# Optimization experiments

Hardware: AMD Instinct MI355X
Metric: run time of the kernel (lower is better)

The kernel has to match this reference:

```python
import jax, jax.numpy as jnp
import numpy as np

D_MODEL = 256; D_FC = 1024; N_LEVELS = 4; N_HEADS = 8; N_POINTS = 4
D_HEAD = D_MODEL // N_HEADS
SPATIAL = np.array([[100, 100], [50, 50], [25, 25], [13, 13]], dtype=np.int64)
S_TOTAL = int((SPATIAL[:, 0] * SPATIAL[:, 1]).sum())  # 13294
BATCH = 2


def setup_inputs() -> dict:
    key = jax.random.key(0)
    ks = jax.random.split(key, 16)

    def lin(k, fi, fo):
        s = 1.0 / np.sqrt(fi)
        kw, kb = jax.random.split(k)
        W = jax.random.uniform(kw, (fi, fo), jnp.float32, -s, s)
        b = jax.random.uniform(kb, (fo,), jnp.float32, -s, s)
        return W, b

    W_off, b_off = lin(ks[0], D_MODEL, N_HEADS * N_LEVELS * N_POINTS * 2)
    W_attn, b_attn = lin(ks[1], D_MODEL, N_HEADS * N_LEVELS * N_POINTS)
    W_val, b_val = lin(ks[2], D_MODEL, D_MODEL)
    W_out, b_out = lin(ks[3], D_MODEL, D_MODEL)
    W1, b1 = lin(ks[4], D_MODEL, D_FC)
    W2, b2 = lin(ks[5], D_FC, D_MODEL)
    src = jax.random.normal(ks[6], (BATCH, S_TOTAL, D_MODEL), jnp.float32)
    pos = jax.random.normal(ks[7], (BATCH, S_TOTAL, D_MODEL), jnp.float32)
    reference_points = jax.random.uniform(ks[8], (BATCH, S_TOTAL, N_LEVELS, 2), jnp.float32)
    level_start_index = np.concatenate([[0], np.cumsum(SPATIAL[:, 0] * SPATIAL[:, 1])[:-1]]).astype(np.int64)
    return dict(src=src, pos=pos, reference_points=reference_points,
                spatial_shapes=SPATIAL, level_start_index=level_start_index,
                W_off=W_off, b_off=b_off, W_attn=W_attn, b_attn=b_attn,
                W_val=W_val, b_val=b_val, W_out=W_out, b_out=b_out,
                ln1_g=jnp.ones(D_MODEL, jnp.float32), ln1_b=jnp.zeros(D_MODEL, jnp.float32),
                W1=W1, b1=b1, W2=W2, b2=b2,
                ln2_g=jnp.ones(D_MODEL, jnp.float32), ln2_b=jnp.zeros(D_MODEL, jnp.float32))


def layernorm(x, g, b, eps=1e-5):
    mu = x.mean(-1, keepdims=True)
    var = ((x - mu) ** 2).mean(-1, keepdims=True)
    return (x - mu) * jax.lax.rsqrt(var + eps) * g + b


def ms_deform_attn(query, value_in, ref_pts, shapes,
                   W_off, b_off, W_attn, b_attn, W_val, b_val, W_out, b_out):
    N, Lq, _ = query.shape
    value = (value_in @ W_val + b_val).reshape(N, -1, N_HEADS, D_HEAD)
    off = (query @ W_off + b_off).reshape(N, Lq, N_HEADS, N_LEVELS, N_POINTS, 2)
    attn = (query @ W_attn + b_attn).reshape(N, Lq, N_HEADS, N_LEVELS * N_POINTS)
    attn = jax.nn.softmax(attn, -1).reshape(N, Lq, N_HEADS, N_LEVELS, N_POINTS)
    # offset normalizer is (W_l, H_l) per level
    norm = jnp.array([[w, h] for (h, w) in shapes], dtype=query.dtype)
    loc = ref_pts[:, :, None, :, None, :] + off / norm[None, None, None, :, None, :]
    out = jnp.zeros((N, Lq, N_HEADS, D_HEAD), query.dtype)
    start = 0
    for l, (H_, W_) in enumerate(shapes):
        v = value[:, start:start + H_ * W_].transpose(0, 2, 1, 3)  # [N, heads, HW, d]
        start += H_ * W_
        loc_l = loc[:, :, :, l]  # [N, Lq, heads, P, 2]
        # grid_sample(align_corners=False, padding_mode='zeros'): pixel = loc*size - 0.5
        px = loc_l[..., 0] * W_ - 0.5
        py = loc_l[..., 1] * H_ - 0.5
        x0 = jnp.floor(px); y0 = jnp.floor(py)
        wx = (px - x0)[..., None]; wy = (py - y0)[..., None]
        x0i = x0.astype(jnp.int32); y0i = y0.astype(jnp.int32)

        def samp(xi, yi):
            valid = (xi >= 0) & (xi < W_) & (yi >= 0) & (yi < H_)
            idx = jnp.clip(yi, 0, H_ - 1) * W_ + jnp.clip(xi, 0, W_ - 1)  # [N,Lq,heads,P]
            idx = idx.transpose(0, 2, 1, 3).reshape(N, N_HEADS, Lq * N_POINTS, 1)
            g = jnp.take_along_axis(v, idx, axis=2)  # [N,heads,Lq*P,d]
            g = g.reshape(N, N_HEADS, Lq, N_POINTS, D_HEAD).transpose(0, 2, 1, 3, 4)
            return g * valid[..., None]

        val = (samp(x0i, y0i) * (1 - wx) * (1 - wy)
               + samp(x0i + 1, y0i) * wx * (1 - wy)
               + samp(x0i, y0i + 1) * (1 - wx) * wy
               + samp(x0i + 1, y0i + 1) * wx * wy)  # [N,Lq,heads,P,d]
        out = out + (val * attn[:, :, :, l, :, None]).sum(3)
    return out.reshape(N, Lq, D_MODEL) @ W_out + b_out


def reference(src, pos, reference_points, spatial_shapes, level_start_index,
              W_off, b_off, W_attn, b_attn, W_val, b_val, W_out, b_out,
              ln1_g, ln1_b, W1, b1, W2, b2, ln2_g, ln2_b):
    shapes = [(int(spatial_shapes[l, 0]), int(spatial_shapes[l, 1])) for l in range(N_LEVELS)]
    q = src + pos
    attn_out = ms_deform_attn(q, src, reference_points, shapes,
                              W_off, b_off, W_attn, b_attn, W_val, b_val, W_out, b_out)
    x = layernorm(src + attn_out, ln1_g, ln1_b)  # dropout is identity in eval
    ffn = jax.nn.relu(x @ W1 + b1) @ W2 + b2
    return layernorm(x + ffn, ln2_g, ln2_b)
```

## Files before the change

kernel.cpp:

```cpp
#include <hip/hip_runtime.h>
#include <hip/hip_bf16.h>

#define DM 256
#define STOT 13294
#define MTOT (2 * STOT)

using bf16 = __hip_bfloat16;
typedef __attribute__((ext_vector_type(8))) short short8;
typedef __attribute__((ext_vector_type(4))) float floatx4;

#define GLDS16(g, l) __builtin_amdgcn_global_load_lds( \
    (const __attribute__((address_space(1))) void*)(g), \
    (__attribute__((address_space(3))) void*)(l), 16, 0, 0)

__device__ __forceinline__ float bu2f(unsigned u) { return __uint_as_float(u << 16); }
__device__ __forceinline__ unsigned short f2bu(float f) {
    union { bf16 h; unsigned short u; } c; c.h = __float2bfloat16(f); return c.u;
}

__global__ void detect_dtype(const unsigned* g1, int* flag) {
    if (threadIdx.x == 0 && blockIdx.x == 0)
        *flag = (g1[0] == 0x3F800000u) ? 1 : 0;
}

struct PW { const void* W[6]; const void* B[10]; };

__global__ void prep_weights(PW a, bf16* __restrict__ WT, float* __restrict__ bf,
                             const int* __restrict__ flag) {
    const long id = (long)blockIdx.x * 256 + threadIdx.x;
    const bool f32in = (*flag != 0);
    const int sz[6]  = {65536, 65536, 32768, 65536, 262144, 262144};
    const int Ns[6]  = {256, 256, 128, 256, 1024, 256};
    const int Ksh[6] = {8, 8, 8, 8, 8, 10};
    if (id < 753664) {
        long e = id; int j = 0;
        while (e >= sz[j]) { e -= sz[j]; ++j; }
        const int n = (int)(e >> Ksh[j]);
        const int k = (int)(e & ((1 << Ksh[j]) - 1));
        const size_t src = (size_t)k * Ns[j] + n;
        float v = f32in ? ((const float*)a.W[j])[src] : __bfloat162float(((const bf16*)a.W[j])[src]);
        WT[id] = __float2bfloat16(v);
    } else if (id < 753664 + 3200) {
        long e = id - 753664; int j = 0;
        const int bsz[10] = {256, 256, 128, 256, 1024, 256, 256, 256, 256, 256};
        while (e >= bsz[j]) { e -= bsz[j]; ++j; }
        float v = f32in ? ((const float*)a.B[j])[e] : __bfloat162float(((const bf16*)a.B[j])[e]);
        bf[id - 753664] = v;
    }
}

__global__ void prep_act(const void* __restrict__ src, const void* __restrict__ pos,
                         bf16* __restrict__ sbf, bf16* __restrict__ qbf,
                         const int* __restrict__ flag) {
    const long i = ((long)blockIdx.x * 256 + threadIdx.x) * 8;
    if (i >= (long)MTOT * DM) return;
    unsigned short ps[8], pq[8];
    if (*flag) {
        const float* s = (const float*)src + i;
        const float* p = (const float*)pos + i;
        float4 a0 = *(const float4*)s, a1 = *(const float4*)(s + 4);
        float4 b0 = *(const float4*)p, b1 = *(const float4*)(p + 4);
        const float av[8] = {a0.x, a0.y, a0.z, a0.w, a1.x, a1.y, a1.z, a1.w};
        const float bv[8] = {b0.x, b0.y, b0.z, b0.w, b1.x, b1.y, b1.z, b1.w};
#pragma unroll
        for (int j = 0; j < 8; ++j) { ps[j] = f2bu(av[j]); pq[j] = f2bu(av[j] + bv[j]); }
    } else {
        const unsigned short* s = (const unsigned short*)src + i;
        const unsigned short* p = (const unsigned short*)pos + i;
        uint4 a = *(const uint4*)s, b = *(const uint4*)p;
        const unsigned* ua = (const unsigned*)&a;
        const unsigned* ub = (const unsigned*)&b;
#pragma unroll
        for (int j = 0; j < 4; ++j) {
            float a0 = bu2f(ua[j] & 0xffffu), a1 = bu2f(ua[j] >> 16);
            float b0 = bu2f(ub[j] & 0xffffu), b1 = bu2f(ub[j] >> 16);
            ps[j * 2] = f2bu(a0); ps[j * 2 + 1] = f2bu(a1);
            pq[j * 2] = f2bu(a0 + b0); pq[j * 2 + 1] = f2bu(a1 + b1);
        }
    }
    *(uint4*)((unsigned short*)sbf + i) = *(const uint4*)ps;
    *(uint4*)((unsigned short*)qbf + i) = *(const uint4*)pq;
}

template<bool RELU>
__global__ __launch_bounds__(256, 4)
void gemm_bf16(const bf16* __restrict__ A0, const bf16* __restrict__ A1, int n_a0,
               const bf16* __restrict__ WT, const float* __restrict__ bias,
               bf16* __restrict__ C0, bf16* __restrict__ C1, bf16* __restrict__ C2,
               int M, int N, int K, int ldc0) {
    __shared__ __align__(16) bf16 sh[16384];
    const int t = threadIdx.x;
    const int wave = t >> 6, lane = t & 63;
    const int bm = blockIdx.y * 128, bn = blockIdx.x * 128;
    const bf16* __restrict__ A = (bn < n_a0) ? A0 : A1;
    const int wm = (wave >> 1) * 64, wn = (wave & 1) * 64;
    const int l15 = lane & 15, quad = lane >> 4;
    const int srow = lane >> 2, sko = (lane & 3) * 8;

    floatx4 acc[4][4];
#pragma unroll
    for (int i = 0; i < 4; ++i)
#pragma unroll
        for (int j = 0; j < 4; ++j) acc[i][j] = (floatx4)0.f;

    const int nb = K >> 5;
#pragma unroll
    for (int rh = 0; rh < 2; ++rh) {
        const int rbase = rh * 64 + wave * 16;
        const int gm = min(bm + rbase + srow, M - 1);
        GLDS16(A + (size_t)gm * K + sko, &sh[rbase * 32]);
        GLDS16(WT + (size_t)(bn + rbase + srow) * K + sko, &sh[8192 + rbase * 32]);
    }
    for (int i = 0; i < nb; ++i) {
        __syncthreads();
        if (i + 1 < nb) {
            const int k0 = (i + 1) << 5;
            const int bo = ((i + 1) & 1) * 4096;
#pragma unroll
            for (int rh = 0; rh < 2; ++rh) {
                const int rbase = rh * 64 + wave * 16;
                const int gm = min(bm + rbase + srow, M - 1);
                GLDS16(A + (size_t)gm * K + k0 + sko, &sh[bo + rbase * 32]);
                GLDS16(WT + (size_t)(bn + rbase + srow) * K + k0 + sko, &sh[8192 + bo + rbase * 32]);
            }
        }
        const int bo = (i & 1) * 4096;
        short8 af[4], bfr[4];
#pragma unroll
        for (int mi = 0; mi < 4; ++mi)
            af[mi] = *(const short8*)&sh[bo + (wm + mi * 16 + l15) * 32 + quad * 8];
#pragma unroll
        for (int nj = 0; nj < 4; ++nj)
            bfr[nj] = *(const short8*)&sh[8192 + bo + (wn + nj * 16 + l15) * 32 + quad * 8];
#pragma unroll
        for (int mi = 0; mi < 4; ++mi)
#pragma unroll
            for (int nj = 0; nj < 4; ++nj)
                acc[mi][nj] = __builtin_amdgcn_mfma_f32_16x16x32_bf16(bfr[nj], af[mi], acc[mi][nj], 0, 0, 0);
    }

    bf16* C = C0; int coloff = bn, ldc = ldc0;
    if (C1 != nullptr && bn >= 256) {
        if (C2 != nullptr && bn >= 512) { C = C2; coloff = bn - 512; ldc = 128; }
        else                            { C = C1; coloff = bn - 256; ldc = 256; }
    }
    float4 bv4[4];
#pragma unroll
    for (int nj = 0; nj < 4; ++nj)
        bv4[nj] = *(const float4*)&bias[bn + wn + nj * 16 + quad * 4];
#pragma unroll
    for (int mi = 0; mi < 4; ++mi) {
        const int gm = bm + wm + mi * 16 + l15;
        if (gm >= M) continue;
#pragma unroll
        for (int nj = 0; nj < 4; ++nj) {
            const float bb[4] = {bv4[nj].x, bv4[nj].y, bv4[nj].z, bv4[nj].w};
            unsigned short pk[4];
#pragma unroll
            for (int r = 0; r < 4; ++r) {
                float v = acc[mi][nj][r] + bb[r];
                if (RELU) v = fmaxf(v, 0.f);
                pk[r] = f2bu(v);
            }
            *(uint2*)&C[(size_t)gm * ldc + coloff + wn + nj * 16 + quad * 4] = *(const uint2*)pk;
        }
    }
}

__global__ void softmax16(bf16* __restrict__ a, int total) {
    const int i = blockIdx.x * 256 + threadIdx.x;
    if (i >= total) return;
    unsigned short* p = (unsigned short*)(a + (size_t)i * 16);
    uint4 r0 = *(const uint4*)p, r1 = *(const uint4*)(p + 8);
    float w[16];
    const unsigned* u0 = (const unsigned*)&r0;
    const unsigned* u1 = (const unsigned*)&r1;
#pragma unroll
    for (int j = 0; j < 4; ++j) {
        w[j * 2] = bu2f(u0[j] & 0xffffu); w[j * 2 + 1] = bu2f(u0[j] >> 16);
        w[8 + j * 2] = bu2f(u1[j] & 0xffffu); w[8 + j * 2 + 1] = bu2f(u1[j] >> 16);
    }
    float mx = -1e30f;
#pragma unroll
    for (int j = 0; j < 16; ++j) mx = fmaxf(mx, w[j]);
    float s = 0.f;
#pragma unroll
    for (int j = 0; j < 16; ++j) { w[j] = __expf(w[j] - mx); s += w[j]; }
    const float inv = 1.f / s;
    unsigned short pk[16];
#pragma unroll
    for (int j = 0; j < 16; ++j) pk[j] = f2bu(w[j] * inv);
    *(uint4*)p = *(const uint4*)pk;
    *(uint4*)(p + 8) = *(const uint4*)(pk + 8);
}

__device__ __forceinline__ void corner(const bf16* __restrict__ base, int xi, int yi,
                                       int W_, int H_, float wgt, float* acc) {
    const bool valid = (xi >= 0) & (xi < W_) & (yi >= 0) & (yi < H_);
    const int xc = min(max(xi, 0), W_ - 1);
    const int yc = min(max(yi, 0), H_ - 1);
    const ushort4 v = *(const ushort4*)(base + (size_t)(yc * W_ + xc) * DM);
    const float m = valid ? wgt : 0.f;
    acc[0] += m * bu2f(v.x); acc[1] += m * bu2f(v.y);
    acc[2] += m * bu2f(v.z); acc[3] += m * bu2f(v.w);
}

__global__ void deform_sample(const bf16* __restrict__ value, const bf16* __restrict__ off,
                              const bf16* __restrict__ attw, const void* __restrict__ refp,
                              bf16* __restrict__ out, const int* __restrict__ flag) {
    const int t = threadIdx.x;
    const int q = blockIdx.x * 4 + (t >> 6);
    const int ln = t & 63;
    const int h = ln >> 3, dg = ln & 7;
    const int b = (q >= STOT) ? 1 : 0;

    float w[16];
    {
        const unsigned short* wp = (const unsigned short*)(attw + (size_t)q * 128 + h * 16);
        uint4 r0 = *(const uint4*)wp, r1 = *(const uint4*)(wp + 8);
        const unsigned* u0 = (const unsigned*)&r0;
        const unsigned* u1 = (const unsigned*)&r1;
#pragma unroll
        for (int j = 0; j < 4; ++j) {
            w[j * 2] = bu2f(u0[j] & 0xffffu); w[j * 2 + 1] = bu2f(u0[j] >> 16);
            w[8 + j * 2] = bu2f(u1[j] & 0xffffu); w[8 + j * 2 + 1] = bu2f(u1[j] >> 16);
        }
    }
    float of[32];
    {
        const unsigned short* op = (const unsigned short*)(off + (size_t)q * 256 + h * 32);
#pragma unroll
        for (int c = 0; c < 4; ++c) {
            uint4 r = *(const uint4*)(op + c * 8);
            const unsigned* u = (const unsigned*)&r;
#pragma unroll
            for (int j = 0; j < 4; ++j) {
                of[c * 8 + j * 2] = bu2f(u[j] & 0xffffu);
                of[c * 8 + j * 2 + 1] = bu2f(u[j] >> 16);
            }
        }
    }
    float rxy[8];
    if (*flag) {
        const float* rp = (const float*)refp + (size_t)q * 8;
        float4 r0 = *(const float4*)rp, r1 = *(const float4*)(rp + 4);
        rxy[0] = r0.x; rxy[1] = r0.y; rxy[2] = r0.z; rxy[3] = r0.w;
        rxy[4] = r1.x; rxy[5] = r1.y; rxy[6] = r1.z; rxy[7] = r1.w;
    } else {
        const unsigned short* rp = (const unsigned short*)refp + (size_t)q * 8;
        uint4 r = *(const uint4*)rp;
        const unsigned* u = (const unsigned*)&r;
#pragma unroll
        for (int j = 0; j < 4; ++j) {
            rxy[j * 2] = bu2f(u[j] & 0xffffu); rxy[j * 2 + 1] = bu2f(u[j] >> 16);
        }
    }

    const int Hs4[4] = {100, 50, 25, 13};
    const int Ls[4] = {0, 10000, 12500, 13125};
    const bf16* vb = value + (size_t)(b * STOT) * DM + h * 32 + dg * 4;

    float acc[4] = {0.f, 0.f, 0.f, 0.f};
#pragma unroll
    for (int l = 0; l < 4; ++l) {
        const int W_ = Hs4[l], H_ = Hs4[l];
        const bf16* base = vb + (size_t)Ls[l] * DM;
        const float fw = (float)W_, fh = (float)H_;
#pragma unroll
        for (int p = 0; p < 4; ++p) {
            const float px = rxy[l * 2] * fw + of[(l * 4 + p) * 2] - 0.5f;
            const float py = rxy[l * 2 + 1] * fh + of[(l * 4 + p) * 2 + 1] - 0.5f;
            const float x0f = floorf(px), y0f = floorf(py);
            const float wx = px - x0f, wy = py - y0f;
            const int x0 = (int)x0f, y0 = (int)y0f;
            const float aw = w[l * 4 + p];
            const float ex = 1.f - wx, ey = 1.f - wy;
            corner(base, x0, y0, W_, H_, ex * ey * aw, acc);
            corner(base, x0 + 1, y0, W_, H_, wx * ey * aw, acc);
            corner(base, x0, y0 + 1, W_, H_, ex * wy * aw, acc);
            corner(base, x0 + 1, y0 + 1, W_, H_, wx * wy * aw, acc);
        }
    }
    unsigned short pk[4] = {f2bu(acc[0]), f2bu(acc[1]), f2bu(acc[2]), f2bu(acc[3])};
    *(ushort4*)((unsigned short*)out + (size_t)q * 256 + h * 32 + dg * 4) = *(const ushort4*)pk;
}

__global__ __launch_bounds__(512, 1)
void out_ln1(const bf16* __restrict__ vsamp, const bf16* __restrict__ srcbf,
             const bf16* __restrict__ WoT, const float* __restrict__ bo_f,
             const float* __restrict__ g1, const float* __restrict__ be1,
             bf16* __restrict__ vx, int M) {
    __shared__ __align__(16) bf16 Bs[8 * 4096];
    const int t = threadIdx.x, wave = t >> 6, lane = t & 63;
    const int l15 = lane & 15, quad = lane >> 4;
    const int srow = lane >> 2, sko = (lane & 3) * 8;
    const int bm = blockIdx.x * 128;
    const int mrow = bm + wave * 16 + l15;
    const int mc = min(mrow, M - 1);

    short8 af[8];
#pragma unroll
    for (int kk = 0; kk < 8; ++kk)
        af[kk] = *(const short8*)(vsamp + (size_t)mc * 256 + kk * 32 + quad * 8);

    floatx4 acc[16];
#pragma unroll
    for (int i = 0; i < 16; ++i) acc[i] = (floatx4)0.f;

    for (int nc = 0; nc < 2; ++nc) {
        __syncthreads();
#pragma unroll
        for (int rr = 0; rr < 8; ++rr)
            GLDS16(WoT + (size_t)(nc * 128 + rr * 16 + srow) * 256 + wave * 32 + sko,
                   &Bs[wave * 4096 + rr * 512]);
        __syncthreads();
#pragma unroll
        for (int kk = 0; kk < 8; ++kk)
#pragma unroll
            for (int nj = 0; nj < 8; ++nj) {
                short8 bfr = *(const short8*)&Bs[kk * 4096 + (nj * 16 + l15) * 32 + quad * 8];
                acc[nc * 8 + nj] = __builtin_amdgcn_mfma_f32_16x16x32_bf16(bfr, af[kk], acc[nc * 8 + nj], 0, 0, 0);
            }
    }

    float s = 0.f;
#pragma unroll
    for (int nj = 0; nj < 16; ++nj) {
        const int n = nj * 16 + quad * 4;
        const float4 bo = *(const float4*)&bo_f[n];
        const uint2 ru = *(const uint2*)(srcbf + (size_t)mc * 256 + n);
        const float rs[4] = {bu2f(ru.x & 0xffffu), bu2f(ru.x >> 16), bu2f(ru.y & 0xffffu), bu2f(ru.y >> 16)};
        const float bb[4] = {bo.x, bo.y, bo.z, bo.w};
#pragma unroll
        for (int r = 0; r < 4; ++r) { acc[nj][r] += bb[r] + rs[r]; s += acc[nj][r]; }
    }
    s += __shfl_xor(s, 16, 64); s += __shfl_xor(s, 32, 64);
    const float mean = s * (1.f / 256.f);
    float s2 = 0.f;
#pragma unroll
    for (int nj = 0; nj < 16; ++nj)
#pragma unroll
        for (int r = 0; r < 4; ++r) { const float c = acc[nj][r] - mean; s2 += c * c; }
    s2 += __shfl_xor(s2, 16, 64); s2 += __shfl_xor(s2, 32, 64);
    const float rstd = rsqrtf(s2 * (1.f / 256.f) + 1e-5f);
    if (mrow < M) {
#pragma unroll
        for (int nj = 0; nj < 16; ++nj) {
            const int n = nj * 16 + quad * 4;
            const float4 g = *(const float4*)&g1[n];
            const float4 b = *(const float4*)&be1[n];
            const float gg[4] = {g.x, g.y, g.z, g.w}, bb[4] = {b.x, b.y, b.z, b.w};
            unsigned short pk[4];
#pragma unroll
            for (int r = 0; r < 4; ++r) pk[r] = f2bu((acc[nj][r] - mean) * rstd * gg[r] + bb[r]);
            *(uint2*)&vx[(size_t)mrow * 256 + n] = *(const uint2*)pk;
        }
    }
}

__global__ __launch_bounds__(256, 2)
void ffn_ln2(const bf16* __restrict__ vx, const bf16* __restrict__ W1T, const bf16* __restrict__ W2T,
             const float* __restrict__ b1f, const float* __restrict__ b2f,
             const float* __restrict__ g2, const float* __restrict__ be2,
             void* __restrict__ outp, const int* __restrict__ flag, int M) {
    __shared__ __align__(16) bf16 Bs1[16384];
    __shared__ __align__(16) bf16 Bs2[8192];
    __shared__ __align__(16) bf16 Hs[64 * 136];
    __shared__ float2 red[128];
    const int t = threadIdx.x, wv = t >> 6, lane = t & 63;
    const int l15 = lane & 15, quad = lane >> 4;
    const int g = wv & 1, nh = wv >> 1;
    const int srow = lane >> 2, sko = (lane & 3) * 8;
    const int bm = blockIdx.x * 64;

    int mrow[2], mc[2];
#pragma unroll
    for (int mi = 0; mi < 2; ++mi) {
        mrow[mi] = bm + g * 32 + mi * 16 + l15;
        mc[mi] = min(mrow[mi], M - 1);
    }
    short8 af[2][8];
#pragma unroll
    for (int mi = 0; mi < 2; ++mi)
#pragma unroll
        for (int kk = 0; kk < 8; ++kk)
            af[mi][kk] = *(const short8*)(vx + (size_t)mc[mi] * 256 + kk * 32 + quad * 8);

    floatx4 acc2[2][8];
#pragma unroll
    for (int mi = 0; mi < 2; ++mi)
#pragma unroll
        for (int nj = 0; nj < 8; ++nj) acc2[mi][nj] = (floatx4)0.f;

    for (int ch = 0; ch < 8; ++ch) {
        floatx4 acc1[2][4];
#pragma unroll
        for (int mi = 0; mi < 2; ++mi)
#pragma unroll
            for (int nj = 0; nj < 4; ++nj) acc1[mi][nj] = (floatx4)0.f;
#pragma unroll
        for (int ks = 0; ks < 2; ++ks) {
            __syncthreads();
#pragma unroll
            for (int j = 0; j < 8; ++j)
                GLDS16(W1T + (size_t)(ch * 128 + j * 16 + srow) * 256 + ks * 128 + wv * 32 + sko,
                       &Bs1[wv * 4096 + j * 512]);
            __syncthreads();
#pragma unroll
            for (int kk = 0; kk < 4; ++kk) {
                short8 bfr[4];
#pragma unroll
                for (int nj = 0; nj < 4; ++nj)
                    bfr[nj] = *(const short8*)&Bs1[kk * 4096 + (nh * 64 + nj * 16 + l15) * 32 + quad * 8];
#pragma unroll
                for (int mi = 0; mi < 2; ++mi)
#pragma unroll
                    for (int nj = 0; nj < 4; ++nj)
                        acc1[mi][nj] = __builtin_amdgcn_mfma_f32_16x16x32_bf16(bfr[nj], af[mi][ks * 4 + kk], acc1[mi][nj], 0, 0, 0);
            }
        }
#pragma unroll
        for (int mi = 0; mi < 2; ++mi)
#pragma unroll
            for (int nj = 0; nj < 4; ++nj) {
                const int kl = nh * 64 + nj * 16 + quad * 4;
                const float4 bb = *(const float4*)&b1f[ch * 128 + kl];
                const float bv[4] = {bb.x, bb.y, bb.z, bb.w};
                unsigned short pk[4];
#pragma unroll
                for (int r = 0; r < 4; ++r) pk[r] = f2bu(fmaxf(acc1[mi][nj][r] + bv[r], 0.f));
                *(uint2*)&Hs[(g * 32 + mi * 16 + l15) * 136 + kl] = *(const uint2*)pk;
            }
#pragma unroll
        for (int p = 0; p < 4; ++p) {
            __syncthreads();
#pragma unroll
            for (int j = 0; j < 4; ++j)
                GLDS16(W2T + (size_t)(wv * 64 + j * 16 + srow) * 1024 + ch * 128 + p * 32 + sko,
                       &Bs2[(wv * 64 + j * 16) * 32]);
            __syncthreads();
            short8 ah[2];
#pragma unroll
            for (int mi = 0; mi < 2; ++mi)
                ah[mi] = *(const short8*)&Hs[(g * 32 + mi * 16 + l15) * 136 + p * 32 + quad * 8];
#pragma unroll
            for (int nj = 0; nj < 8; ++nj) {
                short8 bfr = *(const short8*)&Bs2[(nh * 128 + nj * 16 + l15) * 32 + quad * 8];
#pragma unroll
                for (int mi = 0; mi < 2; ++mi)
                    acc2[mi][nj] = __builtin_amdgcn_mfma_f32_16x16x32_bf16(bfr, ah[mi], acc2[mi][nj], 0, 0, 0);
            }
        }
    }

    float sm[2] = {0.f, 0.f}, sq[2] = {0.f, 0.f};
#pragma unroll
    for (int mi = 0; mi < 2; ++mi)
#pragma unroll
        for (int nj = 0; nj < 8; ++nj) {
            const int n = nh * 128 + nj * 16 + quad * 4;
            const float4 bo = *(const float4*)&b2f[n];
            const uint2 ru = *(const uint2*)(vx + (size_t)mc[mi] * 256 + n);
            const float rs[4] = {bu2f(ru.x & 0xffffu), bu2f(ru.x >> 16), bu2f(ru.y & 0xffffu), bu2f(ru.y >> 16)};
            const float bb[4] = {bo.x, bo.y, bo.z, bo.w};
#pragma unroll
            for (int r = 0; r < 4; ++r) {
                const float v = acc2[mi][nj][r] + bb[r] + rs[r];
                acc2[mi][nj][r] = v; sm[mi] += v; sq[mi] += v * v;
            }
        }
#pragma unroll
    for (int mi = 0; mi < 2; ++mi) {
        sm[mi] += __shfl_xor(sm[mi], 16, 64); sm[mi] += __shfl_xor(sm[mi], 32, 64);
        sq[mi] += __shfl_xor(sq[mi], 16, 64); sq[mi] += __shfl_xor(sq[mi], 32, 64);
    }
    __syncthreads();
    if (quad == 0) {
#pragma unroll
        for (int mi = 0; mi < 2; ++mi)
            red[((nh * 2 + g) * 2 + mi) * 16 + l15] = make_float2(sm[mi], sq[mi]);
    }
    __syncthreads();
    const bool f32o = (*flag != 0);
#pragma unroll
    for (int mi = 0; mi < 2; ++mi) {
        const float2 o = red[(((1 - nh) * 2 + g) * 2 + mi) * 16 + l15];
        const float ts = sm[mi] + o.x, tq = sq[mi] + o.y;
        const float mean = ts * (1.f / 256.f);
        const float var = tq * (1.f / 256.f) - mean * mean;
        const float rstd = rsqrtf(var + 1e-5f);
        if (mrow[mi] < M) {
#pragma unroll
            for (int nj = 0; nj < 8; ++nj) {
                const int n = nh * 128 + nj * 16 + quad * 4;
                const float4 gv = *(const float4*)&g2[n];
                const float4 bv = *(const float4*)&be2[n];
                const float gg[4] = {gv.x, gv.y, gv.z, gv.w}, bb[4] = {bv.x, bv.y, bv.z, bv.w};
                float y[4];
#pragma unroll
                for (int r = 0; r < 4; ++r) y[r] = (acc2[mi][nj][r] - mean) * rstd * gg[r] + bb[r];
                if (f32o) {
                    float4 ov = {y[0], y[1], y[2], y[3]};
                    *(float4*)((float*)outp + (size_t)mrow[mi] * 256 + n) = ov;
                } else {
                    unsigned short pk[4] = {f2bu(y[0]), f2bu(y[1]), f2bu(y[2]), f2bu(y[3])};
                    *(uint2*)((bf16*)outp + (size_t)mrow[mi] * 256 + n) = *(const uint2*)pk;
                }
            }
        }
    }
}

extern "C" void kernel_launch(void* const* d_in, const int* in_sizes, int n_in,
                              void* d_out, int out_size, void* d_ws, size_t ws_size,
                              hipStream_t stream) {
    const void* src   = d_in[0];
    const void* pos   = d_in[1];
    const void* refp  = d_in[2];
    const void* W_off = d_in[5];
    const void* b_off = d_in[6];
    const void* W_att = d_in[7];
    const void* b_att = d_in[8];
    const void* W_val = d_in[9];
    const void* b_val = d_in[10];
    const void* W_out = d_in[11];
    const void* b_out = d_in[12];
    const void* ln1g  = d_in[13];
    const void* ln1b  = d_in[14];
    const void* W1    = d_in[15];
    const void* b1    = d_in[16];
    const void* W2    = d_in[17];
    const void* b2    = d_in[18];
    const void* ln2g  = d_in[19];
    const void* ln2b  = d_in[20];

    const size_t M = MTOT;
    bf16* src_bf = (bf16*)d_ws;
    bf16* q_bf   = src_bf + M * 256;
    bf16* v_val  = src_bf + M * 512;
    bf16* v_off  = src_bf + M * 768;
    bf16* v_attn = src_bf + M * 1024;
    bf16* v_samp = src_bf + M * 1152;
    bf16* v_x    = src_bf + M * 1408;
    bf16* WT     = src_bf + M * 1664;
    float* biasf = (float*)(WT + 753664);
    int* flag    = (int*)(biasf + 3200);

    dim3 blk(256);
    const int mg = (MTOT + 127) / 128;

    detect_dtype<<<1, 64, 0, stream>>>((const unsigned*)ln1g, flag);

    PW pw;
    pw.W[0] = W_val; pw.W[1] = W_off; pw.W[2] = W_att; pw.W[3] = W_out; pw.W[4] = W1; pw.W[5] = W2;
    pw.B[0] = b_val; pw.B[1] = b_off; pw.B[2] = b_att; pw.B[3] = b_out; pw.B[4] = b1; pw.B[5] = b2;
    pw.B[6] = ln1g;  pw.B[7] = ln1b;  pw.B[8] = ln2g;  pw.B[9] = ln2b;
    prep_weights<<<(753664 + 3200 + 255) / 256, blk, 0, stream>>>(pw, WT, biasf, flag);
    prep_act<<<(int)((M * 256 / 8 + 255) / 256), blk, 0, stream>>>(src, pos, src_bf, q_bf, flag);

    gemm_bf16<false><<<dim3(5, mg), blk, 0, stream>>>(src_bf, q_bf, 256, WT, biasf,
                                                      v_val, v_off, v_attn, MTOT, 640, 256, 256);
    softmax16<<<(MTOT * 8 + 255) / 256, blk, 0, stream>>>(v_attn, MTOT * 8);
    deform_sample<<<MTOT / 4, blk, 0, stream>>>(v_val, v_off, v_attn, refp, v_samp, flag);
    out_ln1<<<mg, dim3(512), 0, stream>>>(v_samp, src_bf, WT + 163840, biasf + 640,
                                          biasf + 2176, biasf + 2432, v_x, MTOT);
    ffn_ln2<<<(MTOT + 63) / 64, blk, 0, stream>>>(v_x, WT + 229376, WT + 491520,
                                                  biasf + 896, biasf + 1920,
                                                  biasf + 2688, biasf + 2944,
                                                  d_out, flag, MTOT);
}
```

Before: 312.7 us.

## Precompute bilinear corner indices and weights in LDS before gathering

The sampling kernel now runs in two phases. First, each thread computes the clamped corner byte offsets and masked bilinear-times-attention weights for one (query, head, level, point) and stores them in shared memory. Then each lane gathers value rows using those precomputed offsets with FMA accumulation. This removes the eightfold redundant coordinate math, since every dg lane previously recomputed the same positions, and it shrinks the register footprint. The cost is LDS traffic, a block barrier, and 32-bit byte offsets that assume the value buffer stays under 4 GB.

```diff
diff --git a/kernel.cpp b/kernel.cpp
--- a/kernel.cpp
+++ b/kernel.cpp
@@ -194,94 +194,90 @@
     *(uint4*)(p + 8) = *(const uint4*)(pk + 8);
 }
 
-__device__ __forceinline__ void corner(const bf16* __restrict__ base, int xi, int yi,
-                                       int W_, int H_, float wgt, float* acc) {
-    const bool valid = (xi >= 0) & (xi < W_) & (yi >= 0) & (yi < H_);
-    const int xc = min(max(xi, 0), W_ - 1);
-    const int yc = min(max(yi, 0), H_ - 1);
-    const ushort4 v = *(const ushort4*)(base + (size_t)(yc * W_ + xc) * DM);
-    const float m = valid ? wgt : 0.f;
-    acc[0] += m * bu2f(v.x); acc[1] += m * bu2f(v.y);
-    acc[2] += m * bu2f(v.z); acc[3] += m * bu2f(v.w);
-}
-
-__global__ void deform_sample(const bf16* __restrict__ value, const bf16* __restrict__ off,
-                              const bf16* __restrict__ attw, const void* __restrict__ refp,
-                              bf16* __restrict__ out, const int* __restrict__ flag) {
+__global__ __launch_bounds__(256)
+void deform_sample(const bf16* __restrict__ value, const bf16* __restrict__ off,
+                   const bf16* __restrict__ attw, const void* __restrict__ refp,
+                   bf16* __restrict__ out, const int* __restrict__ flag) {
+    __shared__ int4   sIdx[512];
+    __shared__ float4 sWt[512];
     const int t = threadIdx.x;
-    const int q = blockIdx.x * 4 + (t >> 6);
-    const int ln = t & 63;
+    const bool f32r = (*flag != 0);
+
+#pragma unroll
+    for (int r = 0; r < 2; ++r) {
+        const int e = t + r * 256;
+        const int ql = e >> 7, rem = e & 127;
+        const int h = rem & 7, j = rem >> 3;
+        const int l = j >> 2;
+        const int q = blockIdx.x * 4 + ql;
+        const int b = (q >= STOT) ? 1 : 0;
+        const int Ws4[4] = {100, 50, 25, 13};
+        const int Ls4[4] = {0, 10000, 12500, 13125};
+
+        const unsigned op = *(const unsigned*)((const unsigned short*)off + (size_t)q * 256 + h * 32 + j * 2);
+        const float ox = bu2f(op & 0xffffu), oy = bu2f(op >> 16);
+        const float aw = bu2f(((const unsigned short*)attw)[(size_t)q * 128 + h * 16 + j]);
+        float rx, ry;
+        if (f32r) {
+            const float* rp = (const float*)refp + (size_t)q * 8 + l * 2;
+            rx = rp[0]; ry = rp[1];
+        } else {
+            const unsigned short* rp = (const unsigned short*)refp + (size_t)q * 8 + l * 2;
+            rx = bu2f(rp[0]); ry = bu2f(rp[1]);
+        }
+        const int W_ = Ws4[l];
+        const float fw = (float)W_;
+        const float px = rx * fw + ox - 0.5f;
+        const float py = ry * fw + oy - 0.5f;
+        const float x0f = floorf(px), y0f = floorf(py);
+        const float wx = px - x0f, wy = py - y0f;
+        const int x0 = (int)x0f, y0 = (int)y0f;
+        const float ex = 1.f - wx, ey = 1.f - wy;
+        const int rowb = b * STOT + Ls4[l];
+        const int xs[2] = {x0, x0 + 1}, ys[2] = {y0, y0 + 1};
+        const float fx[2] = {ex, wx}, fy[2] = {ey, wy};
+        int idxv[4]; float wv[4];
+#pragma unroll
+        for (int cy = 0; cy < 2; ++cy)
+#pragma unroll
+            for (int cx = 0; cx < 2; ++cx) {
+                const int xi = xs[cx], yi = ys[cy];
+                const bool valid = (xi >= 0) & (xi < W_) & (yi >= 0) & (yi < W_);
+                const int xc = min(max(xi, 0), W_ - 1);
+                const int yc = min(max(yi, 0), W_ - 1);
+                idxv[cy * 2 + cx] = (rowb + yc * W_ + xc) << 9;
+                wv[cy * 2 + cx] = valid ? fx[cx] * fy[cy] * aw : 0.f;
+            }
+        const int slot = ql * 128 + rem;
+        sIdx[slot] = make_int4(idxv[0], idxv[1], idxv[2], idxv[3]);
+        sWt[slot] = make_float4(wv[0], wv[1], wv[2], wv[3]);
+    }
+    __syncthreads();
+
+    const int ql = t >> 6, ln = t & 63;
     const int h = ln >> 3, dg = ln & 7;
-    const int b = (q >= STOT) ? 1 : 0;
-
-    float w[16];
-    {
-        const unsigned short* wp = (const unsigned short*)(attw + (size_t)q * 128 + h * 16);
-        uint4 r0 = *(const uint4*)wp, r1 = *(const uint4*)(wp + 8);
-        const unsigned* u0 = (const unsigned*)&r0;
-        const unsigned* u1 = (const unsigned*)&r1;
-#pragma unroll
-        for (int j = 0; j < 4; ++j) {
-            w[j * 2] = bu2f(u0[j] & 0xffffu); w[j * 2 + 1] = bu2f(u0[j] >> 16);
-            w[8 + j * 2] = bu2f(u1[j] & 0xffffu); w[8 + j * 2 + 1] = bu2f(u1[j] >> 16);
-        }
-    }
-    float of[32];
-    {
-        const unsigned short* op = (const unsigned short*)(off + (size_t)q * 256 + h * 32);
+    const int q = blockIdx.x * 4 + ql;
+    const char* vbytes = (const char*)value;
+    const unsigned laneoff = (unsigned)((h * 32 + dg * 4) * 2);
+    const int sbase = ql * 128 + h;
+    float a0 = 0.f, a1 = 0.f, a2 = 0.f, a3 = 0.f;
+#pragma unroll 4
+    for (int j = 0; j < 16; ++j) {
+        const int4 iv = sIdx[sbase + j * 8];
+        const float4 wv = sWt[sbase + j * 8];
+        const int iarr[4] = {iv.x, iv.y, iv.z, iv.w};
+        const float warr[4] = {wv.x, wv.y, wv.z, wv.w};
 #pragma unroll
         for (int c = 0; c < 4; ++c) {
-            uint4 r = *(const uint4*)(op + c * 8);
-            const unsigned* u = (const unsigned*)&r;
-#pragma unroll
-            for (int j = 0; j < 4; ++j) {
-                of[c * 8 + j * 2] = bu2f(u[j] & 0xffffu);
-                of[c * 8 + j * 2 + 1] = bu2f(u[j] >> 16);
-            }
-        }
-    }
-    float rxy[8];
-    if (*flag) {
-        const float* rp = (const float*)refp + (size_t)q * 8;
-        float4 r0 = *(const float4*)rp, r1 = *(const float4*)(rp + 4);
-        rxy[0] = r0.x; rxy[1] = r0.y; rxy[2] = r0.z; rxy[3] = r0.w;
-        rxy[4] = r1.x; rxy[5] = r1.y; rxy[6] = r1.z; rxy[7] = r1.w;
-    } else {
-        const unsigned short* rp = (const unsigned short*)refp + (size_t)q * 8;
-        uint4 r = *(const uint4*)rp;
-        const unsigned* u = (const unsigned*)&r;
-#pragma unroll
-        for (int j = 0; j < 4; ++j) {
-            rxy[j * 2] = bu2f(u[j] & 0xffffu); rxy[j * 2 + 1] = bu2f(u[j] >> 16);
-        }
-    }
-
-    const int Hs4[4] = {100, 50, 25, 13};
-    const int Ls[4] = {0, 10000, 12500, 13125};
-    const bf16* vb = value + (size_t)(b * STOT) * DM + h * 32 + dg * 4;
-
-    float acc[4] = {0.f, 0.f, 0.f, 0.f};
-#pragma unroll
-    for (int l = 0; l < 4; ++l) {
-        const int W_ = Hs4[l], H_ = Hs4[l];
-        const bf16* base = vb + (size_t)Ls[l] * DM;
-        const float fw = (float)W_, fh = (float)H_;
-#pragma unroll
-        for (int p = 0; p < 4; ++p) {
-            const float px = rxy[l * 2] * fw + of[(l * 4 + p) * 2] - 0.5f;
-            const float py = rxy[l * 2 + 1] * fh + of[(l * 4 + p) * 2 + 1] - 0.5f;
-            const float x0f = floorf(px), y0f = floorf(py);
-            const float wx = px - x0f, wy = py - y0f;
-            const int x0 = (int)x0f, y0 = (int)y0f;
-            const float aw = w[l * 4 + p];
-            const float ex = 1.f - wx, ey = 1.f - wy;
-            corner(base, x0, y0, W_, H_, ex * ey * aw, acc);
-            corner(base, x0 + 1, y0, W_, H_, wx * ey * aw, acc);
-            corner(base, x0, y0 + 1, W_, H_, ex * wy * aw, acc);
-            corner(base, x0 + 1, y0 + 1, W_, H_, wx * wy * aw, acc);
-        }
-    }
-    unsigned short pk[4] = {f2bu(acc[0]), f2bu(acc[1]), f2bu(acc[2]), f2bu(acc[3])};
+            const unsigned bo = (unsigned)iarr[c] + laneoff;
+            const uint2 v = *(const uint2*)(vbytes + bo);
+            a0 = fmaf(warr[c], __uint_as_float(v.x << 16), a0);
+            a1 = fmaf(warr[c], __uint_as_float(v.x & 0xffff0000u), a1);
+            a2 = fmaf(warr[c], __uint_as_float(v.y << 16), a2);
+            a3 = fmaf(warr[c], __uint_as_float(v.y & 0xffff0000u), a3);
+        }
+    }
+    unsigned short pk[4] = {f2bu(a0), f2bu(a1), f2bu(a2), f2bu(a3)};
     *(ushort4*)((unsigned short*)out + (size_t)q * 256 + h * 32 + dg * 4) = *(const ushort4*)pk;
 }
 
```

New measurement: 326.6 us. 4.5% more time.
